# Optimization experiments

Measured on AMD Instinct MI355X. Metric: run time of the kernel, lower is better.

## Reference

```python
import jax, jax.numpy as jnp
import numpy as np

INPUT_SIZE = 512
HIDDEN_SIZE = 1024
BATCH = 16384


def setup_inputs() -> dict:
    key = jax.random.key(0)
    ks = jax.random.split(key, 11)
    s_x = 1.0 / np.sqrt(INPUT_SIZE)
    s_h = 1.0 / np.sqrt(HIDDEN_SIZE)
    inp = {
        "x": jax.random.normal(ks[0], (BATCH, INPUT_SIZE), dtype=jnp.float32),
        "hidden": jax.random.normal(ks[1], (BATCH, HIDDEN_SIZE), dtype=jnp.float32),
        # Linear weights stored as (in, out) for x @ W
        "Wxr": jax.random.uniform(ks[2], (INPUT_SIZE, HIDDEN_SIZE), jnp.float32, -s_x, s_x),
        "bxr": jax.random.uniform(ks[3], (HIDDEN_SIZE,), jnp.float32, -s_x, s_x),
        "Whr": jax.random.uniform(ks[4], (HIDDEN_SIZE, HIDDEN_SIZE), jnp.float32, -s_h, s_h),
        "Wxz": jax.random.uniform(ks[5], (INPUT_SIZE, HIDDEN_SIZE), jnp.float32, -s_x, s_x),
        "bxz": jax.random.uniform(ks[6], (HIDDEN_SIZE,), jnp.float32, -s_x, s_x),
        "Whz": jax.random.uniform(ks[7], (HIDDEN_SIZE, HIDDEN_SIZE), jnp.float32, -s_h, s_h),
        "Wxh": jax.random.uniform(ks[8], (INPUT_SIZE, HIDDEN_SIZE), jnp.float32, -s_x, s_x),
        "bxh": jax.random.uniform(ks[9], (HIDDEN_SIZE,), jnp.float32, -s_x, s_x),
        "Whh": jax.random.uniform(ks[10], (HIDDEN_SIZE, HIDDEN_SIZE), jnp.float32, -s_h, s_h),
    }
    return inp


def reference(x, hidden, Wxr, bxr, Whr, Wxz, bxz, Whz, Wxh, bxh, Whh):
    # GRU cell, single timestep.
    r = jax.nn.sigmoid(x @ Wxr + bxr + hidden @ Whr)          # reset gate (B,H)
    z = jax.nn.sigmoid(x @ Wxz + bxz + hidden @ Whz)          # update gate (B,H)
    h_cand = jnp.tanh(x @ Wxh + bxh + (r * hidden) @ Whh)     # candidate (B,H)
    return z * hidden + (1.0 - z) * h_cand
```

## Files before the change

### kernel.cpp

```cpp
#include <hip/hip_runtime.h>

typedef unsigned short u16;
typedef unsigned int u32;
typedef __bf16 bf16x8 __attribute__((ext_vector_type(8)));
typedef float f32x4 __attribute__((ext_vector_type(4)));

#define B_ROWS 16384
#define K1 1536

__device__ __forceinline__ u16 f2bf(float f) {
  u32 u = __float_as_uint(f);
  u = (u + 0x7fffu + ((u >> 16) & 1u)) >> 16;
  return (u16)u;
}
__device__ __forceinline__ float bf2f(u16 b) {
  return __uint_as_float(((u32)b) << 16);
}
__device__ __forceinline__ void gload_lds16(const void* g, void* l) {
  __builtin_amdgcn_global_load_lds((const __attribute__((address_space(1))) void*)g,
                                   (__attribute__((address_space(3))) void*)l,
                                   16, 0, 0);
}

__global__ void cvt_xh(const float* __restrict__ x, const float* __restrict__ h,
                       u16* __restrict__ xh) {
  const int iv = blockIdx.x * 256 + threadIdx.x;
  const int row = iv / 384;
  const int col = (iv - row * 384) * 4;
  const float* src = (col < 512) ? x + (size_t)row * 512 + col
                                 : h + (size_t)row * 1024 + (col - 512);
  float4 v = *(const float4*)src;
  u32 a = (u32)f2bf(v.x) | ((u32)f2bf(v.y) << 16);
  u32 b = (u32)f2bf(v.z) | ((u32)f2bf(v.w) << 16);
  *(uint2*)(xh + (size_t)row * 1536 + col) = make_uint2(a, b);
}

__global__ void transpose_cvt6(const float* __restrict__ Wxr, const float* __restrict__ Whr,
                               const float* __restrict__ Wxz, const float* __restrict__ Whz,
                               const float* __restrict__ Wxh, const float* __restrict__ Whh,
                               u16* __restrict__ W1t, u16* __restrict__ W2t) {
  __shared__ float tile[32][33];
  const int z = blockIdx.z;
  const float* W;
  u16* T;
  int Ks, koff, roff;
  switch (z) {
    case 0:  W = Wxr; T = W1t; Ks = 512;  koff = 0;   roff = 0;    break;
    case 1:  W = Whr; T = W1t; Ks = 1024; koff = 512; roff = 0;    break;
    case 2:  W = Wxz; T = W1t; Ks = 512;  koff = 0;   roff = 1024; break;
    case 3:  W = Whz; T = W1t; Ks = 1024; koff = 512; roff = 1024; break;
    case 4:  W = Wxh; T = W2t; Ks = 512;  koff = 0;   roff = 0;    break;
    default: W = Whh; T = W2t; Ks = 1024; koff = 512; roff = 0;    break;
  }
  const int bx = blockIdx.x, by = blockIdx.y;
  if (by * 32 >= Ks) return;
  const int tx = threadIdx.x, ty = threadIdx.y;
#pragma unroll
  for (int r = 0; r < 32; r += 8)
    tile[ty + r][tx] = W[(size_t)(by * 32 + ty + r) * 1024 + bx * 32 + tx];
  __syncthreads();
#pragma unroll
  for (int r = 0; r < 32; r += 8)
    T[(size_t)(roff + bx * 32 + ty + r) * K1 + koff + by * 32 + tx] = f2bf(tile[tx][ty + r]);
}

struct Src {
  const u16 *a0, *a1, *b0, *b1;
  int sa0, sa1, sb0, sb1, tsplit;
};

__device__ __forceinline__ const u16* gsrc(const u16* p0, const u16* p1, int s0, int s1,
                                           int tsplit, int t, int grow) {
  return (t < tsplit) ? p0 + (size_t)grow * s0 + t * 64
                      : p1 + (size_t)grow * s1 + (t - tsplit) * 64;
}

__device__ __forceinline__ void stage_half(const u16* p0, const u16* p1, int s0, int s1,
                                           int tsplit, int t, int rowbase, int h,
                                           char* matB, int c, int tid, int kswz) {
  char* lds = matB + c * 32768 + h * 16384 + ((tid >> 6) << 10);
  const int r = tid >> 3;
  const u16* g0 = gsrc(p0, p1, s0, s1, tsplit, t, rowbase + h * 128 + r) + kswz;
  const u16* g1 = gsrc(p0, p1, s0, s1, tsplit, t, rowbase + h * 128 + 64 + r) + kswz;
  gload_lds16(g0, lds);
  gload_lds16(g1, lds + 8192);
}

#define STAGE_A(t_, c_, h_) \
  stage_half(S.a0, S.a1, S.sa0, S.sa1, S.tsplit, (t_), brow, (h_), AsB, (c_), tid, kswz)
#define STAGE_B(t_, c_, h_) \
  stage_half(S.b0, S.b1, S.sb0, S.sb1, S.tsplit, (t_), bcol, (h_), BsB, (c_), tid, kswz)

__device__ __forceinline__ void gemm256(const Src& S, int nt, int brow, int bcol,
                                        u16* AsU, u16* BsU, f32x4 acc[8][4]) {
  const int tid = threadIdx.x;
  const int l = tid & 63;
  const int wid = tid >> 6;
  const int wr = wid >> 2, wc = wid & 3;
  const int lr = l & 15, kq = l >> 4;
  const int swzB = (lr & 7) * 16;
  const int kswz = ((tid & 7) ^ ((tid >> 3) & 7)) * 8;
  char* AsB = (char*)AsU;
  char* BsB = (char*)BsU;
  const int colK0 = (kq * 16) ^ swzB;
  const int colK1 = (64 + kq * 16) ^ swzB;
  int aRow[8], bRow[4];
#pragma unroll
  for (int m = 0; m < 8; ++m) aRow[m] = (wr * 128 + m * 16 + lr) * 128;
#pragma unroll
  for (int n = 0; n < 4; ++n) bRow[n] = (wc * 64 + n * 16 + lr) * 128;

  STAGE_A(0, 0, 0);
  STAGE_A(0, 0, 1);
  STAGE_B(0, 0, 0);
  STAGE_B(0, 0, 1);
  if (1 < nt) STAGE_A(1, 1, 0);
  asm volatile("s_waitcnt vmcnt(2)" ::: "memory");
  __builtin_amdgcn_s_barrier();
  asm volatile("" ::: "memory");

  for (int t = 0; t < nt; ++t) {
    const int c = t & 1;
    const int cb = c << 15;
    bf16x8 a[4][2], b[4][2];
#pragma unroll
    for (int m = 0; m < 4; ++m) {
      a[m][0] = *(const bf16x8*)(AsB + cb + aRow[m] + colK0);
      a[m][1] = *(const bf16x8*)(AsB + cb + aRow[m] + colK1);
    }
#pragma unroll
    for (int n = 0; n < 2; ++n) {
      b[n][0] = *(const bf16x8*)(BsB + cb + bRow[n] + colK0);
      b[n][1] = *(const bf16x8*)(BsB + cb + bRow[n] + colK1);
    }
    if (t + 1 < nt) STAGE_A(t + 1, c ^ 1, 1);
    __builtin_amdgcn_s_barrier();
    asm volatile("s_waitcnt lgkmcnt(0)" ::: "memory");
    __builtin_amdgcn_sched_barrier(0);
    __builtin_amdgcn_s_setprio(1);
#pragma unroll
    for (int kk = 0; kk < 2; ++kk)
#pragma unroll
      for (int m = 0; m < 4; ++m)
#pragma unroll
        for (int n = 0; n < 2; ++n)
          acc[m][n] = __builtin_amdgcn_mfma_f32_16x16x32_bf16(a[m][kk], b[n][kk], acc[m][n], 0, 0, 0);
    __builtin_amdgcn_s_setprio(0);
    __builtin_amdgcn_s_barrier();
    asm volatile("" ::: "memory");
#pragma unroll
    for (int n = 2; n < 4; ++n) {
      b[n][0] = *(const bf16x8*)(BsB + cb + bRow[n] + colK0);
      b[n][1] = *(const bf16x8*)(BsB + cb + bRow[n] + colK1);
    }
    if (t + 1 < nt) STAGE_B(t + 1, c ^ 1, 0);
    __builtin_amdgcn_s_barrier();
    asm volatile("s_waitcnt lgkmcnt(0)" ::: "memory");
    __builtin_amdgcn_sched_barrier(0);
    __builtin_amdgcn_s_setprio(1);
#pragma unroll
    for (int kk = 0; kk < 2; ++kk)
#pragma unroll
      for (int m = 0; m < 4; ++m)
#pragma unroll
        for (int n = 2; n < 4; ++n)
          acc[m][n] = __builtin_amdgcn_mfma_f32_16x16x32_bf16(a[m][kk], b[n][kk], acc[m][n], 0, 0, 0);
    __builtin_amdgcn_s_setprio(0);
    __builtin_amdgcn_s_barrier();
    asm volatile("" ::: "memory");
#pragma unroll
    for (int m = 0; m < 4; ++m) {
      a[m][0] = *(const bf16x8*)(AsB + cb + aRow[m + 4] + colK0);
      a[m][1] = *(const bf16x8*)(AsB + cb + aRow[m + 4] + colK1);
    }
    if (t + 1 < nt) STAGE_B(t + 1, c ^ 1, 1);
    __builtin_amdgcn_s_barrier();
    asm volatile("s_waitcnt lgkmcnt(0)" ::: "memory");
    __builtin_amdgcn_sched_barrier(0);
    __builtin_amdgcn_s_setprio(1);
#pragma unroll
    for (int kk = 0; kk < 2; ++kk)
#pragma unroll
      for (int m = 0; m < 4; ++m)
#pragma unroll
        for (int n = 2; n < 4; ++n)
          acc[m + 4][n] = __builtin_amdgcn_mfma_f32_16x16x32_bf16(a[m][kk], b[n][kk], acc[m + 4][n], 0, 0, 0);
    __builtin_amdgcn_s_setprio(0);
    __builtin_amdgcn_s_barrier();
    asm volatile("" ::: "memory");
    if (t + 2 < nt) STAGE_A(t + 2, c, 0);
    __builtin_amdgcn_s_barrier();
    __builtin_amdgcn_s_setprio(1);
#pragma unroll
    for (int kk = 0; kk < 2; ++kk)
#pragma unroll
      for (int m = 0; m < 4; ++m)
#pragma unroll
        for (int n = 0; n < 2; ++n)
          acc[m + 4][n] = __builtin_amdgcn_mfma_f32_16x16x32_bf16(a[m][kk], b[n][kk], acc[m + 4][n], 0, 0, 0);
    __builtin_amdgcn_s_setprio(0);
    if (t + 2 < nt) { asm volatile("s_waitcnt vmcnt(2)" ::: "memory"); }
    else            { asm volatile("s_waitcnt vmcnt(0)" ::: "memory"); }
    __builtin_amdgcn_s_barrier();
    asm volatile("" ::: "memory");
  }
}

__global__ __launch_bounds__(512, 2) void gru_gemm1(
    const u16* __restrict__ xh, const u16* __restrict__ W1t,
    const float* __restrict__ bxr, const float* __restrict__ bxz,
    u16* __restrict__ rhb, u16* __restrict__ zb) {
  __shared__ __align__(16) u16 As[2 * 256 * 64];
  __shared__ __align__(16) u16 Bs[2 * 256 * 64];
  const int orig = blockIdx.x;
  const int slot = orig >> 3;
  const int mt = (orig & 7) + 8 * (slot >> 3);
  const int jt = slot & 7;
  const int brow = mt * 256;
  const int jcol = jt * 256;

  Src S;
  S.a0 = xh;  S.sa0 = K1; S.a1 = xh + 512;  S.sa1 = K1;
  S.b0 = W1t; S.sb0 = K1; S.b1 = W1t + 512; S.sb1 = K1;
  S.tsplit = 8;

  f32x4 acc[8][4] = {};
  gemm256(S, 24, brow, jcol, As, Bs, acc);

  const int l = threadIdx.x & 63;
  const int wid = threadIdx.x >> 6;
  const int wr = wid >> 2, wc = wid & 3;
  const int colb = jcol + wc * 64 + (l & 15);
  const int rowb = brow + wr * 128 + (l >> 4) * 4;
  if (jt < 4) {
#pragma unroll
    for (int n = 0; n < 4; ++n) {
      const int col = colb + n * 16;
      const float bias = bxr[col];
#pragma unroll
      for (int m = 0; m < 8; ++m)
#pragma unroll
        for (int j = 0; j < 4; ++j) {
          const int row = rowb + m * 16 + j;
          const float rg = 1.f / (1.f + __expf(-(acc[m][n][j] + bias)));
          const float hv = bf2f(xh[(size_t)row * K1 + 512 + col]);
          rhb[(size_t)row * 1024 + col] = f2bf(rg * hv);
        }
    }
  } else {
#pragma unroll
    for (int n = 0; n < 4; ++n) {
      const int col = colb + n * 16 - 1024;
      const float bias = bxz[col];
#pragma unroll
      for (int m = 0; m < 8; ++m)
#pragma unroll
        for (int j = 0; j < 4; ++j) {
          const int row = rowb + m * 16 + j;
          const float zg = 1.f / (1.f + __expf(-(acc[m][n][j] + bias)));
          zb[(size_t)row * 1024 + col] = f2bf(zg);
        }
    }
  }
}

__global__ __launch_bounds__(512, 2) void gru_gemm2(
    const u16* __restrict__ xh, const u16* __restrict__ rhb,
    const u16* __restrict__ W2t, const float* __restrict__ bxh,
    const u16* __restrict__ zb, const float* __restrict__ hidden,
    float* __restrict__ out) {
  __shared__ __align__(16) u16 As[2 * 256 * 64];
  __shared__ __align__(16) u16 Bs[2 * 256 * 64];
  const int orig = blockIdx.x;
  const int wg = (orig & 7) * 32 + (orig >> 3);
  const int mt = wg & 63, jt = wg >> 6;
  const int brow = mt * 256;
  const int jcol = jt * 256;

  Src S;
  S.a0 = xh;  S.sa0 = K1; S.a1 = rhb;       S.sa1 = 1024;
  S.b0 = W2t; S.sb0 = K1; S.b1 = W2t + 512; S.sb1 = K1;
  S.tsplit = 8;

  f32x4 acc[8][4] = {};
  gemm256(S, 24, brow, jcol, As, Bs, acc);

  const int l = threadIdx.x & 63;
  const int wid = threadIdx.x >> 6;
  const int wr = wid >> 2, wc = wid & 3;
  const int colb = jcol + wc * 64 + (l & 15);
  const int rowb = brow + wr * 128 + (l >> 4) * 4;
#pragma unroll
  for (int n = 0; n < 4; ++n) {
    const int col = colb + n * 16;
    const float bias = bxh[col];
#pragma unroll
    for (int m = 0; m < 8; ++m)
#pragma unroll
      for (int j = 0; j < 4; ++j) {
        const int row = rowb + m * 16 + j;
        const size_t idx = (size_t)row * 1024 + col;
        const float e = __expf(2.f * (acc[m][n][j] + bias));
        const float hc = 1.f - 2.f / (e + 1.f);
        const float z = bf2f(zb[idx]);
        const float h = hidden[idx];
        out[idx] = z * h + (1.f - z) * hc;
      }
  }
}

extern "C" void kernel_launch(void* const* d_in, const int* in_sizes, int n_in,
                              void* d_out, int out_size, void* d_ws, size_t ws_size,
                              hipStream_t stream) {
  const float* x      = (const float*)d_in[0];
  const float* hidden = (const float*)d_in[1];
  const float* Wxr = (const float*)d_in[2];
  const float* bxr = (const float*)d_in[3];
  const float* Whr = (const float*)d_in[4];
  const float* Wxz = (const float*)d_in[5];
  const float* bxz = (const float*)d_in[6];
  const float* Whz = (const float*)d_in[7];
  const float* Wxh = (const float*)d_in[8];
  const float* bxh = (const float*)d_in[9];
  const float* Whh = (const float*)d_in[10];
  float* out = (float*)d_out;
  (void)in_sizes; (void)n_in; (void)out_size; (void)ws_size;

  char* p = (char*)d_ws;
  u16* xh  = (u16*)p; p += (size_t)B_ROWS * K1 * 2;
  u16* W1t = (u16*)p; p += (size_t)2048 * K1 * 2;
  u16* W2t = (u16*)p; p += (size_t)1024 * K1 * 2;
  u16* rhb = (u16*)p; p += (size_t)B_ROWS * 1024 * 2;
  u16* zb  = (u16*)p; p += (size_t)B_ROWS * 1024 * 2;

  cvt_xh<<<B_ROWS * 384 / 256, 256, 0, stream>>>(x, hidden, xh);
  transpose_cvt6<<<dim3(32, 32, 6), dim3(32, 8), 0, stream>>>(
      Wxr, Whr, Wxz, Whz, Wxh, Whh, W1t, W2t);

  gru_gemm1<<<512, 512, 0, stream>>>(xh, W1t, bxr, bxz, rhb, zb);
  gru_gemm2<<<256, 512, 0, stream>>>(xh, rhb, W2t, bxh, zb, hidden, out);
}
```

Baseline: 265.0 us.

## Precompute GEMM staging offsets and read bf16 hidden in GRU epilogue

```diff
diff --git a/kernel.cpp b/kernel.cpp
--- a/kernel.cpp
+++ b/kernel.cpp
@@ -65,31 +65,10 @@
 }
 
 struct Src {
-  const u16 *a0, *a1, *b0, *b1;
-  int sa0, sa1, sb0, sb1, tsplit;
+  const u16 *A, *B, *A2;
+  u32 sA, sB, sA2;
+  int tsw;
 };
-
-__device__ __forceinline__ const u16* gsrc(const u16* p0, const u16* p1, int s0, int s1,
-                                           int tsplit, int t, int grow) {
-  return (t < tsplit) ? p0 + (size_t)grow * s0 + t * 64
-                      : p1 + (size_t)grow * s1 + (t - tsplit) * 64;
-}
-
-__device__ __forceinline__ void stage_half(const u16* p0, const u16* p1, int s0, int s1,
-                                           int tsplit, int t, int rowbase, int h,
-                                           char* matB, int c, int tid, int kswz) {
-  char* lds = matB + c * 32768 + h * 16384 + ((tid >> 6) << 10);
-  const int r = tid >> 3;
-  const u16* g0 = gsrc(p0, p1, s0, s1, tsplit, t, rowbase + h * 128 + r) + kswz;
-  const u16* g1 = gsrc(p0, p1, s0, s1, tsplit, t, rowbase + h * 128 + 64 + r) + kswz;
-  gload_lds16(g0, lds);
-  gload_lds16(g1, lds + 8192);
-}
-
-#define STAGE_A(t_, c_, h_) \
-  stage_half(S.a0, S.a1, S.sa0, S.sa1, S.tsplit, (t_), brow, (h_), AsB, (c_), tid, kswz)
-#define STAGE_B(t_, c_, h_) \
-  stage_half(S.b0, S.b1, S.sb0, S.sb1, S.tsplit, (t_), bcol, (h_), BsB, (c_), tid, kswz)
 
 __device__ __forceinline__ void gemm256(const Src& S, int nt, int brow, int bcol,
                                         u16* AsU, u16* BsU, f32x4 acc[8][4]) {
@@ -99,9 +78,11 @@
   const int wr = wid >> 2, wc = wid & 3;
   const int lr = l & 15, kq = l >> 4;
   const int swzB = (lr & 7) * 16;
-  const int kswz = ((tid & 7) ^ ((tid >> 3) & 7)) * 8;
+  const int kswzE = ((tid & 7) ^ ((tid >> 3) & 7)) * 8;
+  const int r = tid >> 3;
   char* AsB = (char*)AsU;
   char* BsB = (char*)BsU;
+  const int ldsQ = wid << 10;
   const int colK0 = (kq * 16) ^ swzB;
   const int colK1 = (64 + kq * 16) ^ swzB;
   int aRow[8], bRow[4];
@@ -110,11 +91,30 @@
 #pragma unroll
   for (int n = 0; n < 4; ++n) bRow[n] = (wc * 64 + n * 16 + lr) * 128;
 
-  STAGE_A(0, 0, 0);
-  STAGE_A(0, 0, 1);
-  STAGE_B(0, 0, 0);
-  STAGE_B(0, 0, 1);
-  if (1 < nt) STAGE_A(1, 1, 0);
+  const u16* pA01 = S.A;
+  const u16* pA23 = S.A;
+  u32 offA[4], offB[4];
+#pragma unroll
+  for (int q = 0; q < 4; ++q) {
+    offA[q] = (u32)((brow + q * 64 + r) * S.sA + kswzE) * 2u;
+    offB[q] = (u32)((bcol + q * 64 + r) * S.sB + kswzE) * 2u;
+  }
+
+#define STG_A01(q_, c_) gload_lds16((const char*)pA01 + offA[q_], \
+    AsB + (c_) * 32768 + (q_) * 8192 + ldsQ)
+#define STG_A23(q_, c_) gload_lds16((const char*)pA23 + offA[q_], \
+    AsB + (c_) * 32768 + 16384 + ((q_) - 2) * 8192 + ldsQ)
+#define STG_B(q_, c_)   gload_lds16((const char*)S.B + offB[q_], \
+    BsB + (c_) * 32768 + ((q_) >> 1) * 16384 + ((q_) & 1) * 8192 + ldsQ)
+
+  STG_A01(0, 0); STG_A01(1, 0);
+  STG_A23(2, 0); STG_A23(3, 0);
+  STG_B(0, 0); STG_B(1, 0); STG_B(2, 0); STG_B(3, 0);
+  offA[0] += 128; offA[1] += 128;
+  STG_A01(0, 1); STG_A01(1, 1);
+  offA[0] += 128; offA[1] += 128;
+  offA[2] += 128; offA[3] += 128;
+  offB[0] += 128; offB[1] += 128; offB[2] += 128; offB[3] += 128;
   asm volatile("s_waitcnt vmcnt(2)" ::: "memory");
   __builtin_amdgcn_s_barrier();
   asm volatile("" ::: "memory");
@@ -133,7 +133,7 @@
       b[n][0] = *(const bf16x8*)(BsB + cb + bRow[n] + colK0);
       b[n][1] = *(const bf16x8*)(BsB + cb + bRow[n] + colK1);
     }
-    if (t + 1 < nt) STAGE_A(t + 1, c ^ 1, 1);
+    if (t + 1 < nt) { STG_A23(2, c ^ 1); STG_A23(3, c ^ 1); }
     __builtin_amdgcn_s_barrier();
     asm volatile("s_waitcnt lgkmcnt(0)" ::: "memory");
     __builtin_amdgcn_sched_barrier(0);
@@ -153,7 +153,7 @@
       b[n][0] = *(const bf16x8*)(BsB + cb + bRow[n] + colK0);
       b[n][1] = *(const bf16x8*)(BsB + cb + bRow[n] + colK1);
     }
-    if (t + 1 < nt) STAGE_B(t + 1, c ^ 1, 0);
+    if (t + 1 < nt) { STG_B(0, c ^ 1); STG_B(1, c ^ 1); }
     __builtin_amdgcn_s_barrier();
     asm volatile("s_waitcnt lgkmcnt(0)" ::: "memory");
     __builtin_amdgcn_sched_barrier(0);
@@ -173,7 +173,7 @@
       a[m][0] = *(const bf16x8*)(AsB + cb + aRow[m + 4] + colK0);
       a[m][1] = *(const bf16x8*)(AsB + cb + aRow[m + 4] + colK1);
     }
-    if (t + 1 < nt) STAGE_B(t + 1, c ^ 1, 1);
+    if (t + 1 < nt) { STG_B(2, c ^ 1); STG_B(3, c ^ 1); }
     __builtin_amdgcn_s_barrier();
     asm volatile("s_waitcnt lgkmcnt(0)" ::: "memory");
     __builtin_amdgcn_sched_barrier(0);
@@ -188,7 +188,7 @@
     __builtin_amdgcn_s_setprio(0);
     __builtin_amdgcn_s_barrier();
     asm volatile("" ::: "memory");
-    if (t + 2 < nt) STAGE_A(t + 2, c, 0);
+    if (t + 2 < nt) { STG_A01(0, c); STG_A01(1, c); }
     __builtin_amdgcn_s_barrier();
     __builtin_amdgcn_s_setprio(1);
 #pragma unroll
@@ -203,7 +203,21 @@
     else            { asm volatile("s_waitcnt vmcnt(0)" ::: "memory"); }
     __builtin_amdgcn_s_barrier();
     asm volatile("" ::: "memory");
-  }
+    if (t == S.tsw - 3) {
+      pA01 = S.A2;
+      offA[0] = (u32)((brow + 0 * 64 + r) * S.sA2 + kswzE) * 2u;
+      offA[1] = (u32)((brow + 1 * 64 + r) * S.sA2 + kswzE) * 2u;
+    } else { offA[0] += 128; offA[1] += 128; }
+    if (t == S.tsw - 2) {
+      pA23 = S.A2;
+      offA[2] = (u32)((brow + 2 * 64 + r) * S.sA2 + kswzE) * 2u;
+      offA[3] = (u32)((brow + 3 * 64 + r) * S.sA2 + kswzE) * 2u;
+    } else { offA[2] += 128; offA[3] += 128; }
+    offB[0] += 128; offB[1] += 128; offB[2] += 128; offB[3] += 128;
+  }
+#undef STG_A01
+#undef STG_A23
+#undef STG_B
 }
 
 __global__ __launch_bounds__(512, 2) void gru_gemm1(
@@ -220,9 +234,8 @@
   const int jcol = jt * 256;
 
   Src S;
-  S.a0 = xh;  S.sa0 = K1; S.a1 = xh + 512;  S.sa1 = K1;
-  S.b0 = W1t; S.sb0 = K1; S.b1 = W1t + 512; S.sb1 = K1;
-  S.tsplit = 8;
+  S.A = xh; S.sA = K1; S.B = W1t; S.sB = K1;
+  S.A2 = xh; S.sA2 = K1; S.tsw = 1 << 20;
 
   f32x4 acc[8][4] = {};
   gemm256(S, 24, brow, jcol, As, Bs, acc);
@@ -267,8 +280,7 @@
 __global__ __launch_bounds__(512, 2) void gru_gemm2(
     const u16* __restrict__ xh, const u16* __restrict__ rhb,
     const u16* __restrict__ W2t, const float* __restrict__ bxh,
-    const u16* __restrict__ zb, const float* __restrict__ hidden,
-    float* __restrict__ out) {
+    const u16* __restrict__ zb, float* __restrict__ out) {
   __shared__ __align__(16) u16 As[2 * 256 * 64];
   __shared__ __align__(16) u16 Bs[2 * 256 * 64];
   const int orig = blockIdx.x;
@@ -278,9 +290,8 @@
   const int jcol = jt * 256;
 
   Src S;
-  S.a0 = xh;  S.sa0 = K1; S.a1 = rhb;       S.sa1 = 1024;
-  S.b0 = W2t; S.sb0 = K1; S.b1 = W2t + 512; S.sb1 = K1;
-  S.tsplit = 8;
+  S.A = xh; S.sA = K1; S.B = W2t; S.sB = K1;
+  S.A2 = rhb; S.sA2 = 1024; S.tsw = 8;
 
   f32x4 acc[8][4] = {};
   gemm256(S, 24, brow, jcol, As, Bs, acc);
@@ -303,7 +314,7 @@
         const float e = __expf(2.f * (acc[m][n][j] + bias));
         const float hc = 1.f - 2.f / (e + 1.f);
         const float z = bf2f(zb[idx]);
-        const float h = hidden[idx];
+        const float h = bf2f(xh[(size_t)row * K1 + 512 + col]);
         out[idx] = z * h + (1.f - z) * hc;
       }
   }
@@ -338,5 +349,5 @@
       Wxr, Whr, Wxz, Whz, Wxh, Whh, W1t, W2t);
 
   gru_gemm1<<<512, 512, 0, stream>>>(xh, W1t, bxr, bxz, rhb, zb);
-  gru_gemm2<<<256, 512, 0, stream>>>(xh, rhb, W2t, bxh, zb, hidden, out);
-}
+  gru_gemm2<<<256, 512, 0, stream>>>(xh, rhb, W2t, bxh, zb, out);
+}
```

Result: slower. 270.5 us (+2.1%).
